# Optimization experiments

Hardware: AMD Instinct MI355X
Metric: run time of the kernel (lower is better)

The kernel has to match this reference:

```python
import jax, jax.numpy as jnp
import numpy as np
from jax import lax

B, C, TX, TY = 16, 192, 512, 2048
SEG = 8192 // 256  # segment_frames = 32 (hop length 256)
NEG_INF = -1e9


def setup_inputs() -> dict:
    key = jax.random.key(0)
    ks = jax.random.split(key, 7)
    z = jax.random.normal(ks[0], (B, C, TY), jnp.float32)
    z_p = jax.random.normal(ks[1], (B, C, TY), jnp.float32)
    m_p = jax.random.normal(ks[2], (B, C, TX), jnp.float32)
    logs_p = 0.1 * jax.random.normal(ks[3], (B, C, TX), jnp.float32)
    x_lengths = jax.random.randint(ks[4], (B,), TX // 2, TX + 1, jnp.int32)
    y_lengths = jax.random.randint(ks[5], (B,), TY // 2, TY + 1, jnp.int32)
    rand_u = jax.random.uniform(ks[6], (B,), jnp.float32)
    return dict(z=z, z_p=z_p, m_p=m_p, logs_p=logs_p,
                x_lengths=x_lengths, y_lengths=y_lengths, rand_u=rand_u)


def neg_cent_fn(z_p, m_p, logs_p):
    # sum_c -0.5 * exp(-2 logs)[c,tx] * (z_p[c,ty] - m_p[c,tx])^2 - sum_c logs[c,tx]
    # expanded (z-m)^2 = z^2 - 2 z m + m^2 -> batched GEMMs (same math as broadcast form)
    s = jnp.exp(-2.0 * logs_p)                                 # [B,C,Tx]
    a = jnp.einsum('bct,bcs->bts', -0.5 * z_p * z_p, s)        # [B,Ty,Tx]
    b = jnp.einsum('bct,bcs->bts', z_p, s * m_p)               # [B,Ty,Tx]
    c = jnp.sum(-0.5 * s * m_p * m_p - logs_p, axis=1)         # [B,Tx]
    return a + b + c[:, None, :]


def maximum_path_single(value, t_x, t_y):
    # Monotonic alignment search DP on value [Ty,Tx], valid region [:t_y,:t_x].
    Ty, Tx = value.shape
    tx = jnp.arange(Tx)

    def fwd(v, row):
        v_shift = jnp.concatenate([jnp.full((1,), NEG_INF, v.dtype), v[:-1]])
        dirn = v_shift > v                      # True: best predecessor is tx-1
        v_new = row + jnp.maximum(v, v_shift)
        v_new = jnp.where(tx < t_x, v_new, NEG_INF)
        v_new = jnp.maximum(v_new, NEG_INF)     # clamp accumulation
        return v_new, dirn

    v0 = jnp.where(tx == 0, 0.0, NEG_INF)
    _, dirs = lax.scan(fwd, v0, value)          # dirs [Ty,Tx] bool

    def bwd(idx, j):
        active = j < t_y
        idx = jnp.where(j == t_y - 1, t_x - 1, idx)
        row = jnp.where(active, jnp.zeros((Tx,), value.dtype).at[idx].set(1.0), 0.0)
        idx = jnp.where(active, idx - dirs[j, idx].astype(idx.dtype), idx)
        return idx, row

    _, path_rev = lax.scan(bwd, jnp.int32(0), jnp.arange(Ty - 1, -1, -1))
    return path_rev[::-1]                       # [Ty,Tx] 0/1 path


def rand_slice_segments(z, y_lengths, rand_u):
    t = z.shape[2]
    safe = jnp.minimum(y_lengths, t)
    ids_max = jnp.maximum(safe - SEG, 0)
    ids = (rand_u * (ids_max.astype(jnp.float32) + 1e-8)).astype(jnp.int32)
    zs = jax.vmap(lambda zi, s: lax.dynamic_slice_in_dim(zi, s, SEG, axis=1))(z, ids)
    valid = (jnp.arange(SEG)[None, None, :] < (safe - ids)[:, None, None])
    return zs * valid.astype(z.dtype), ids


def reference(z, z_p, m_p, logs_p, x_lengths, y_lengths, rand_u):
    neg_cent = neg_cent_fn(z_p, m_p, logs_p)                     # [B,Ty,Tx]
    attn = jax.vmap(maximum_path_single)(neg_cent, x_lengths, y_lengths)
    attn = lax.stop_gradient(attn)                               # torch: no_grad + detach
    m_p_a = jnp.einsum('bts,bcs->bct', attn, m_p)                # [B,C,Ty]
    logs_p_a = jnp.einsum('bts,bcs->bct', attn, logs_p)          # [B,C,Ty]
    z_slice, ids_slice = rand_slice_segments(z, y_lengths, rand_u)
    return z_slice, ids_slice, attn, m_p_a, logs_p_a
```

## Files before the change

### kernel.cpp

```cpp
#include <hip/hip_runtime.h>
#include <stdint.h>

#define B_   16
#define C_   192
#define TX_  512
#define TY_  2048
#define K_   384
#define SEG_ 32
#define NEG_INF_ (-1e9f)


__global__ __launch_bounds__(128) void k_prep(const float* __restrict__ mp,
                                              const float* __restrict__ logsp,
                                              float* __restrict__ Bmat,
                                              float* __restrict__ cterm) {
    int b  = blockIdx.y;
    int tx = blockIdx.x * 128 + threadIdx.x;
    const float* mb = mp    + (size_t)b * C_ * TX_ + tx;
    const float* lb = logsp + (size_t)b * C_ * TX_ + tx;
    float* B0 = Bmat + (size_t)b * K_ * TX_ + tx;
    float acc = 0.f;
    for (int c = 0; c < C_; ++c) {
        float lg = lb[(size_t)c * TX_];
        float m  = mb[(size_t)c * TX_];
        float s  = expf(-2.f * lg);
        B0[(size_t)c * TX_]        = s;
        B0[(size_t)(C_ + c) * TX_] = s * m;
        acc += -0.5f * s * m * m - lg;
    }
    cterm[b * TX_ + tx] = acc;
}

__global__ __launch_bounds__(256) void k_gemm(const float* __restrict__ zp,
                                              const float* __restrict__ Bmat,
                                              const float* __restrict__ cterm,
                                              float* __restrict__ ncout) {
    __shared__ float As[16][128];
    __shared__ float Bs[16][128];
    int b  = blockIdx.z;
    int m0 = blockIdx.y * 128;
    int n0 = blockIdx.x * 128;
    int tid = threadIdx.x;
    int tm = tid >> 4;
    int tn = tid & 15;
    const float* zpb = zp   + (size_t)b * C_ * TY_;
    const float* Bb  = Bmat + (size_t)b * K_ * TX_;

    float acc[8][8];
#pragma unroll
    for (int i = 0; i < 8; ++i)
#pragma unroll
        for (int j = 0; j < 8; ++j) acc[i][j] = 0.f;

    int lrow = tid >> 5;
    int lcol = (tid & 31) << 2;

    for (int k0 = 0; k0 < K_; k0 += 16) {
        int ksrc = (k0 < C_) ? k0 : (k0 - C_);
        const float* Ab = zpb + (size_t)(ksrc + lrow) * TY_ + m0 + lcol;
        float4 z0 = *(const float4*)Ab;
        float4 z1 = *(const float4*)(Ab + (size_t)8 * TY_);
        if (k0 < C_) {
            z0.x = -0.5f * z0.x * z0.x; z0.y = -0.5f * z0.y * z0.y;
            z0.z = -0.5f * z0.z * z0.z; z0.w = -0.5f * z0.w * z0.w;
            z1.x = -0.5f * z1.x * z1.x; z1.y = -0.5f * z1.y * z1.y;
            z1.z = -0.5f * z1.z * z1.z; z1.w = -0.5f * z1.w * z1.w;
        }
        const float* Bp = Bb + (size_t)(k0 + lrow) * TX_ + n0 + lcol;
        float4 w0 = *(const float4*)Bp;
        float4 w1 = *(const float4*)(Bp + (size_t)8 * TX_);

        __syncthreads();
        *(float4*)&As[lrow][lcol]     = z0;
        *(float4*)&As[lrow + 8][lcol] = z1;
        *(float4*)&Bs[lrow][lcol]     = w0;
        *(float4*)&Bs[lrow + 8][lcol] = w1;
        __syncthreads();

#pragma unroll
        for (int kk = 0; kk < 16; ++kk) {
            float4 a0 = *(const float4*)&As[kk][tm * 8];
            float4 a1 = *(const float4*)&As[kk][tm * 8 + 4];
            float4 b0 = *(const float4*)&Bs[kk][tn * 8];
            float4 b1 = *(const float4*)&Bs[kk][tn * 8 + 4];
            float a[8]  = {a0.x, a0.y, a0.z, a0.w, a1.x, a1.y, a1.z, a1.w};
            float bb[8] = {b0.x, b0.y, b0.z, b0.w, b1.x, b1.y, b1.z, b1.w};
#pragma unroll
            for (int i = 0; i < 8; ++i)
#pragma unroll
                for (int j = 0; j < 8; ++j)
                    acc[i][j] = fmaf(a[i], bb[j], acc[i][j]);
        }
    }

    float cadd[8];
#pragma unroll
    for (int j = 0; j < 8; ++j) cadd[j] = cterm[b * TX_ + n0 + tn * 8 + j];

#pragma unroll
    for (int i = 0; i < 8; ++i) {
        int row = m0 + tm * 8 + i;
        float* orow = ncout + ((size_t)b * TY_ + row) * TX_ + n0 + tn * 8;
        float4 o0, o1;
        o0.x = acc[i][0] + cadd[0]; o0.y = acc[i][1] + cadd[1];
        o0.z = acc[i][2] + cadd[2]; o0.w = acc[i][3] + cadd[3];
        o1.x = acc[i][4] + cadd[4]; o1.y = acc[i][5] + cadd[5];
        o1.z = acc[i][6] + cadd[6]; o1.w = acc[i][7] + cadd[7];
        *(float4*)orow       = o0;
        *(float4*)(orow + 4) = o1;
    }
}

#define NS_ 14
#define NP_ 7

__global__ __launch_bounds__(512, 1) void k_dp(const float* __restrict__ nc,
                                               const int* __restrict__ xl,
                                               const int* __restrict__ yl,
                                               int* __restrict__ path,
                                               unsigned char* __restrict__ gdirs) {
    extern __shared__ unsigned char slds[];
    float*    stagef   = (float*)slds;
    unsigned* flags    = (unsigned*)(slds + NS_ * 8192);
    unsigned* cons_ctr = flags + NS_;

    int b    = blockIdx.x;
    int tid  = threadIdx.x;
    int w    = tid >> 6;
    int lane = tid & 63;
    int t_x  = xl[b];
    int t_y  = yl[b]; if (t_y > TY_) t_y = TY_;
    const float* ncb = nc + (size_t)b * TY_ * TX_;
    unsigned char* gb = gdirs + (size_t)b * (TY_ * 64);
    int ng = (t_y + 3) >> 2;

    if (tid < NS_ + 1) flags[tid] = 0u;
    __syncthreads();

    if (w != 0) {
        int cv = (int)__hip_atomic_load(cons_ctr, __ATOMIC_ACQUIRE,
                                        __HIP_MEMORY_SCOPE_WORKGROUP);
        for (int g = w - 1; g < ng; g += NP_) {
            while (cv < g - (NS_ - 1)) {
                __builtin_amdgcn_s_sleep(1);
                cv = (int)__hip_atomic_load(cons_ctr, __ATOMIC_ACQUIRE,
                                            __HIP_MEMORY_SCOPE_WORKGROUP);
            }
            int j0 = g * 4;
            float* sb = stagef + (g % NS_) * 2048;
#pragma unroll
            for (int r = 0; r < 4; ++r) {
                const float4* row = (const float4*)(ncb + (size_t)(j0 + r) * TX_);
                float4 q0 = row[2 * lane];
                float4 q1 = row[2 * lane + 1];
                *(float4*)(sb + r * 512 + lane * 4)       = q0;
                *(float4*)(sb + r * 512 + 256 + lane * 4) = q1;
            }
            if (lane == 0)
                __hip_atomic_store(&flags[g % NS_], (unsigned)(g + 1),
                                   __ATOMIC_RELEASE, __HIP_MEMORY_SCOPE_WORKGROUP);
            cv = (int)__hip_atomic_load(cons_ctr, __ATOMIC_ACQUIRE,
                                        __HIP_MEMORY_SCOPE_WORKGROUP);
        }
        return;
    }

    int col0 = lane * 8;
    float v[8];
#pragma unroll
    for (int k = 0; k < 8; ++k) v[k] = (col0 + k == 0) ? 0.f : NEG_INF_;

    const unsigned neg_bits = __float_as_uint(NEG_INF_);
    unsigned fv = 0;
    for (int g = 0; g < ng; ++g) {
        while (fv != (unsigned)(g + 1))
            fv = __hip_atomic_load(&flags[g % NS_], __ATOMIC_ACQUIRE,
                                   __HIP_MEMORY_SCOPE_WORKGROUP);
        unsigned fnx = __hip_atomic_load(&flags[(g + 1) % NS_], __ATOMIC_ACQUIRE,
                                         __HIP_MEMORY_SCOPE_WORKGROUP);
        const float* rowp = stagef + (g % NS_) * 2048;
        unsigned dw = 0u;
#pragma unroll
        for (int r = 0; r < 4; ++r) {
            float4 p0 = *(const float4*)(rowp + r * 512 + lane * 4);
            float4 p1 = *(const float4*)(rowp + r * 512 + 256 + lane * 4);
            float rc[8] = {p0.x, p0.y, p0.z, p0.w, p1.x, p1.y, p1.z, p1.w};
            float left = __uint_as_float(__builtin_amdgcn_update_dpp(
                (int)neg_bits, (int)__float_as_uint(v[7]),
                0x138 , 0xF, 0xF, false));
            unsigned by = 0u;
#pragma unroll
            for (int k = 7; k >= 0; --k) {
                float vs = (k == 0) ? left : v[k - 1];
                if (vs > v[k]) by |= (1u << k);
                v[k] = fmaxf(v[k], vs) + rc[k];
            }
            dw |= by << (8 * r);
        }
        int j0 = g * 4;
        gb[(size_t)(j0    ) * 64 + lane] = (unsigned char)(dw      );
        gb[(size_t)(j0 + 1) * 64 + lane] = (unsigned char)(dw >>  8);
        gb[(size_t)(j0 + 2) * 64 + lane] = (unsigned char)(dw >> 16);
        gb[(size_t)(j0 + 3) * 64 + lane] = (unsigned char)(dw >> 24);
        if (lane == 0)
            __hip_atomic_store(cons_ctr, (unsigned)(g + 1),
                               __ATOMIC_RELEASE, __HIP_MEMORY_SCOPE_WORKGROUP);
        fv = fnx;
    }

    __builtin_amdgcn_s_waitcnt(3952);

    int* pb = path + b * TY_;
    for (int j2 = t_y + lane; j2 < TY_; j2 += 64) pb[j2] = -1;

    unsigned char* swin = (unsigned char*)stagef;
    int j   = t_y - 1;
    int idx = t_x - 1;
    while (j >= 0) {
        int nb = (j + 1 < 64) ? (j + 1) : 64;
        if (lane < nb) {
            const uint4* rp = (const uint4*)(gb + (size_t)(j - lane) * 64);
            uint4 a0 = rp[0], a1 = rp[1], a2 = rp[2], a3 = rp[3];
            uint4* wp = (uint4*)(swin + lane * 64);
            wp[0] = a0; wp[1] = a1; wp[2] = a2; wp[3] = a3;
        }
        if (lane == 0) {
            int r2 = 0;
            while (r2 < nb) {
                int n = nb - r2; if (n > 8) n = 8;
                int Bhi = idx >> 3;
                int Blo = Bhi - 1; if (Blo < 0) Blo = 0;
                unsigned lo8[8], hi8[8];
#pragma unroll
                for (int r = 0; r < 8; ++r) {
                    if (r < n) {
                        lo8[r] = swin[(r2 + r) * 64 + Blo];
                        hi8[r] = swin[(r2 + r) * 64 + Bhi];
                    }
                }
#pragma unroll
                for (int r = 0; r < 8; ++r) {
                    if (r < n) {
                        pb[j - (r2 + r)] = idx;
                        unsigned byte = ((idx >> 3) == Bhi) ? hi8[r] : lo8[r];
                        idx -= (int)((byte >> (idx & 7)) & 1u);
                    }
                }
                r2 += n;
            }
        }
        j -= nb;
    }
}

__global__ __launch_bounds__(256) void k_attn(const int* __restrict__ path,
                                              float* __restrict__ attn) {
    int i   = blockIdx.x * 256 + threadIdx.x;
    int tx0 = (i & 127) << 2;
    int bty = i >> 7;
    int p   = path[bty];
    float4 o;
    o.x = (p == tx0)     ? 1.f : 0.f;
    o.y = (p == tx0 + 1) ? 1.f : 0.f;
    o.z = (p == tx0 + 2) ? 1.f : 0.f;
    o.w = (p == tx0 + 3) ? 1.f : 0.f;
    ((float4*)attn)[i] = o;
}

__global__ __launch_bounds__(256) void k_proj(const int* __restrict__ path,
                                              const float* __restrict__ mp,
                                              const float* __restrict__ logsp,
                                              float* __restrict__ mpa,
                                              float* __restrict__ logsa) {
    int i   = blockIdx.x * 256 + threadIdx.x;
    int ty0 = (i & 511) << 2;
    int bc  = i >> 9;
    int b   = bc / C_;
    const int4 p4 = *(const int4*)(path + b * TY_ + ty0);
    const float* mrow = mp    + (size_t)bc * TX_;
    const float* lrow = logsp + (size_t)bc * TX_;
    float4 mo, lo;
    mo.x = (p4.x >= 0) ? mrow[p4.x] : 0.f;  lo.x = (p4.x >= 0) ? lrow[p4.x] : 0.f;
    mo.y = (p4.y >= 0) ? mrow[p4.y] : 0.f;  lo.y = (p4.y >= 0) ? lrow[p4.y] : 0.f;
    mo.z = (p4.z >= 0) ? mrow[p4.z] : 0.f;  lo.z = (p4.z >= 0) ? lrow[p4.z] : 0.f;
    mo.w = (p4.w >= 0) ? mrow[p4.w] : 0.f;  lo.w = (p4.w >= 0) ? lrow[p4.w] : 0.f;
    ((float4*)mpa)[i]   = mo;
    ((float4*)logsa)[i] = lo;
}

__global__ __launch_bounds__(256) void k_slice(const float* __restrict__ z,
                                               const int* __restrict__ yl,
                                               const float* __restrict__ ru,
                                               float* __restrict__ zs,
                                               float* __restrict__ oid) {
    int b = blockIdx.x;
    int safe = yl[b]; if (safe > TY_) safe = TY_;
    int idsmax = safe - SEG_; if (idsmax < 0) idsmax = 0;
    int ids = (int)(ru[b] * ((float)idsmax + 1e-8f));
    int lim = safe - ids;
    for (int t = threadIdx.x; t < C_ * SEG_; t += 256) {
        int c = t >> 5, k = t & 31;
        zs[b * C_ * SEG_ + t] =
            (k < lim) ? z[((size_t)b * C_ + c) * TY_ + ids + k] : 0.f;
    }
    if (threadIdx.x == 0) oid[b] = (float)ids;
}

extern "C" void kernel_launch(void* const* d_in, const int* in_sizes, int n_in,
                              void* d_out, int out_size, void* d_ws, size_t ws_size,
                              hipStream_t stream) {
    const float* z     = (const float*)d_in[0];
    const float* zp    = (const float*)d_in[1];
    const float* mp    = (const float*)d_in[2];
    const float* logsp = (const float*)d_in[3];
    const int*   xl    = (const int*)d_in[4];
    const int*   yl    = (const int*)d_in[5];
    const float* ru    = (const float*)d_in[6];

    float* out     = (float*)d_out;
    float* o_zs    = out;
    float* o_ids   = out + 98304;
    float* o_attn  = out + 98320;
    float* o_mpa   = out + 16875536;
    float* o_logsa = out + 23166992;

    float*         Bmat  = (float*)d_ws;
    float*         cterm = Bmat + (size_t)B_ * K_ * TX_;
    int*           path  = (int*)(cterm + B_ * TX_);
    unsigned char* gdirs = (unsigned char*)(path + B_ * TY_);

    const int dp_lds = NS_ * 8192 + 64;

    hipFuncSetAttribute((const void*)k_dp,
                        hipFuncAttributeMaxDynamicSharedMemorySize, dp_lds);

    hipLaunchKernelGGL(k_prep, dim3(TX_ / 128, B_), dim3(128), 0, stream,
                       mp, logsp, Bmat, cterm);
    hipLaunchKernelGGL(k_gemm, dim3(TX_ / 128, TY_ / 128, B_), dim3(256), 0, stream,
                       zp, Bmat, cterm, o_attn);
    hipLaunchKernelGGL(k_dp, dim3(B_), dim3(512), dp_lds, stream,
                       o_attn, xl, yl, path, gdirs);
    hipLaunchKernelGGL(k_attn, dim3(B_ * TY_ * TX_ / 4 / 256), dim3(256), 0, stream,
                       path, o_attn);
    hipLaunchKernelGGL(k_proj, dim3(B_ * C_ * TY_ / 4 / 256), dim3(256), 0, stream,
                       path, mp, logsp, o_mpa, o_logsa);
    hipLaunchKernelGGL(k_slice, dim3(B_), dim3(256), 0, stream,
                       z, yl, ru, o_zs, o_ids);
}
```

Measured before the change: 781.7 us.

## Replace flag-based DP staging ring with double-buffered phases and block barriers

The DP kernel's producer/consumer ring (14 slots, per-slot atomic flags, spin-waits) becomes a two-buffer scheme of 32-row phases, synchronised with __syncthreads. Producer waves fill the next 64 KB buffer while the consumer wave runs the DP recurrence on the current one. Direction bits are now stored as one 32-bit word per lane per 4 rows instead of four byte stores, and the backtrack window loads and addressing change to match. This removes fine-grained atomic polling and per-row byte stores, but the consumer now waits at a full barrier every 32 rows and LDS use rises to 128 KB.

```diff
diff --git a/kernel.cpp b/kernel.cpp
--- a/kernel.cpp
+++ b/kernel.cpp
@@ -111,18 +111,16 @@
     }
 }
 
-#define NS_ 14
-#define NP_ 7
+#define NPROD_ 7
 
 __global__ __launch_bounds__(512, 1) void k_dp(const float* __restrict__ nc,
                                                const int* __restrict__ xl,
                                                const int* __restrict__ yl,
                                                int* __restrict__ path,
-                                               unsigned char* __restrict__ gdirs) {
+                                               unsigned* __restrict__ gdirs32) {
     extern __shared__ unsigned char slds[];
-    float*    stagef   = (float*)slds;
-    unsigned* flags    = (unsigned*)(slds + NS_ * 8192);
-    unsigned* cons_ctr = flags + NS_;
+    float* buf0 = (float*)slds;
+    float* buf1 = (float*)(slds + 65536);
 
     int b    = blockIdx.x;
     int tid  = threadIdx.x;
@@ -131,36 +129,34 @@
     int t_x  = xl[b];
     int t_y  = yl[b]; if (t_y > TY_) t_y = TY_;
     const float* ncb = nc + (size_t)b * TY_ * TX_;
-    unsigned char* gb = gdirs + (size_t)b * (TY_ * 64);
-    int ng = (t_y + 3) >> 2;
-
-    if (tid < NS_ + 1) flags[tid] = 0u;
-    __syncthreads();
+    unsigned* gb32 = gdirs32 + (size_t)b * (TY_ / 4) * 64;
+    int nph = (t_y + 31) >> 5;
 
     if (w != 0) {
-        int cv = (int)__hip_atomic_load(cons_ctr, __ATOMIC_ACQUIRE,
-                                        __HIP_MEMORY_SCOPE_WORKGROUP);
-        for (int g = w - 1; g < ng; g += NP_) {
-            while (cv < g - (NS_ - 1)) {
-                __builtin_amdgcn_s_sleep(1);
-                cv = (int)__hip_atomic_load(cons_ctr, __ATOMIC_ACQUIRE,
-                                            __HIP_MEMORY_SCOPE_WORKGROUP);
-            }
-            int j0 = g * 4;
-            float* sb = stagef + (g % NS_) * 2048;
-#pragma unroll
-            for (int r = 0; r < 4; ++r) {
-                const float4* row = (const float4*)(ncb + (size_t)(j0 + r) * TX_);
+        {
+            for (int rr = w - 1; rr < 32; rr += NPROD_) {
+                const float4* row = (const float4*)(ncb + (size_t)rr * TX_);
                 float4 q0 = row[2 * lane];
                 float4 q1 = row[2 * lane + 1];
-                *(float4*)(sb + r * 512 + lane * 4)       = q0;
-                *(float4*)(sb + r * 512 + 256 + lane * 4) = q1;
+                *(float4*)(buf0 + rr * 512 + lane * 4)       = q0;
+                *(float4*)(buf0 + rr * 512 + 256 + lane * 4) = q1;
             }
-            if (lane == 0)
-                __hip_atomic_store(&flags[g % NS_], (unsigned)(g + 1),
-                                   __ATOMIC_RELEASE, __HIP_MEMORY_SCOPE_WORKGROUP);
-            cv = (int)__hip_atomic_load(cons_ctr, __ATOMIC_ACQUIRE,
-                                        __HIP_MEMORY_SCOPE_WORKGROUP);
+        }
+        __syncthreads();
+        for (int p = 0; p < nph; ++p) {
+            if (p + 1 < nph) {
+                float* sb = ((p + 1) & 1) ? buf1 : buf0;
+                int jbase = (p + 1) * 32;
+                for (int rr = w - 1; rr < 32; rr += NPROD_) {
+                    const float4* row =
+                        (const float4*)(ncb + (size_t)(jbase + rr) * TX_);
+                    float4 q0 = row[2 * lane];
+                    float4 q1 = row[2 * lane + 1];
+                    *(float4*)(sb + rr * 512 + lane * 4)       = q0;
+                    *(float4*)(sb + rr * 512 + 256 + lane * 4) = q1;
+                }
+            }
+            __syncthreads();
         }
         return;
     }
@@ -169,43 +165,35 @@
     float v[8];
 #pragma unroll
     for (int k = 0; k < 8; ++k) v[k] = (col0 + k == 0) ? 0.f : NEG_INF_;
-
     const unsigned neg_bits = __float_as_uint(NEG_INF_);
-    unsigned fv = 0;
-    for (int g = 0; g < ng; ++g) {
-        while (fv != (unsigned)(g + 1))
-            fv = __hip_atomic_load(&flags[g % NS_], __ATOMIC_ACQUIRE,
-                                   __HIP_MEMORY_SCOPE_WORKGROUP);
-        unsigned fnx = __hip_atomic_load(&flags[(g + 1) % NS_], __ATOMIC_ACQUIRE,
-                                         __HIP_MEMORY_SCOPE_WORKGROUP);
-        const float* rowp = stagef + (g % NS_) * 2048;
-        unsigned dw = 0u;
-#pragma unroll
-        for (int r = 0; r < 4; ++r) {
-            float4 p0 = *(const float4*)(rowp + r * 512 + lane * 4);
-            float4 p1 = *(const float4*)(rowp + r * 512 + 256 + lane * 4);
-            float rc[8] = {p0.x, p0.y, p0.z, p0.w, p1.x, p1.y, p1.z, p1.w};
-            float left = __uint_as_float(__builtin_amdgcn_update_dpp(
-                (int)neg_bits, (int)__float_as_uint(v[7]),
-                0x138 , 0xF, 0xF, false));
-            unsigned by = 0u;
-#pragma unroll
-            for (int k = 7; k >= 0; --k) {
-                float vs = (k == 0) ? left : v[k - 1];
-                if (vs > v[k]) by |= (1u << k);
-                v[k] = fmaxf(v[k], vs) + rc[k];
+
+    __syncthreads();
+    for (int p = 0; p < nph; ++p) {
+        const float* sb = (p & 1) ? buf1 : buf0;
+#pragma unroll
+        for (int g = 0; g < 8; ++g) {
+            unsigned dw = 0u;
+#pragma unroll
+            for (int r = 0; r < 4; ++r) {
+                const float* rowp = sb + (g * 4 + r) * 512;
+                float4 p0 = *(const float4*)(rowp + lane * 4);
+                float4 p1 = *(const float4*)(rowp + 256 + lane * 4);
+                float rc[8] = {p0.x, p0.y, p0.z, p0.w, p1.x, p1.y, p1.z, p1.w};
+                float left = __uint_as_float(__builtin_amdgcn_update_dpp(
+                    (int)neg_bits, (int)__float_as_uint(v[7]),
+                    0x138 , 0xF, 0xF, false));
+                unsigned by = 0u;
+#pragma unroll
+                for (int k = 7; k >= 0; --k) {
+                    float vs = (k == 0) ? left : v[k - 1];
+                    if (vs > v[k]) by |= (1u << k);
+                    v[k] = fmaxf(v[k], vs) + rc[k];
+                }
+                dw |= by << (8 * r);
             }
-            dw |= by << (8 * r);
-        }
-        int j0 = g * 4;
-        gb[(size_t)(j0    ) * 64 + lane] = (unsigned char)(dw      );
-        gb[(size_t)(j0 + 1) * 64 + lane] = (unsigned char)(dw >>  8);
-        gb[(size_t)(j0 + 2) * 64 + lane] = (unsigned char)(dw >> 16);
-        gb[(size_t)(j0 + 3) * 64 + lane] = (unsigned char)(dw >> 24);
-        if (lane == 0)
-            __hip_atomic_store(cons_ctr, (unsigned)(g + 1),
-                               __ATOMIC_RELEASE, __HIP_MEMORY_SCOPE_WORKGROUP);
-        fv = fnx;
+            gb32[(p * 8 + g) * 64 + lane] = dw;
+        }
+        __syncthreads();
     }
 
     __builtin_amdgcn_s_waitcnt(3952);
@@ -213,43 +201,49 @@
     int* pb = path + b * TY_;
     for (int j2 = t_y + lane; j2 < TY_; j2 += 64) pb[j2] = -1;
 
-    unsigned char* swin = (unsigned char*)stagef;
+    const unsigned char* gb = (const unsigned char*)gb32;
+    unsigned char* swin = (unsigned char*)buf0;
     int j   = t_y - 1;
     int idx = t_x - 1;
     while (j >= 0) {
-        int nb = (j + 1 < 64) ? (j + 1) : 64;
-        if (lane < nb) {
-            const uint4* rp = (const uint4*)(gb + (size_t)(j - lane) * 64);
-            uint4 a0 = rp[0], a1 = rp[1], a2 = rp[2], a3 = rp[3];
+        int wbase = (j & ~3) - 60; if (wbase < 0) wbase = 0;
+        {
+            const uint4* rp = (const uint4*)(gb + (size_t)(wbase >> 2) * 256);
+            uint4 a0 = rp[lane * 4 + 0];
+            uint4 a1 = rp[lane * 4 + 1];
+            uint4 a2 = rp[lane * 4 + 2];
+            uint4 a3 = rp[lane * 4 + 3];
             uint4* wp = (uint4*)(swin + lane * 64);
             wp[0] = a0; wp[1] = a1; wp[2] = a2; wp[3] = a3;
         }
         if (lane == 0) {
-            int r2 = 0;
-            while (r2 < nb) {
-                int n = nb - r2; if (n > 8) n = 8;
+            while (j >= wbase) {
+                int n = j - wbase + 1; if (n > 8) n = 8;
                 int Bhi = idx >> 3;
                 int Blo = Bhi - 1; if (Blo < 0) Blo = 0;
                 unsigned lo8[8], hi8[8];
 #pragma unroll
                 for (int r = 0; r < 8; ++r) {
                     if (r < n) {
-                        lo8[r] = swin[(r2 + r) * 64 + Blo];
-                        hi8[r] = swin[(r2 + r) * 64 + Bhi];
+                        int jr  = j - r;
+                        int off = ((jr - wbase) >> 2) * 256 + (jr & 3);
+                        lo8[r] = swin[off + Blo * 4];
+                        hi8[r] = swin[off + Bhi * 4];
                     }
                 }
 #pragma unroll
                 for (int r = 0; r < 8; ++r) {
                     if (r < n) {
-                        pb[j - (r2 + r)] = idx;
+                        pb[j - r] = idx;
                         unsigned byte = ((idx >> 3) == Bhi) ? hi8[r] : lo8[r];
                         idx -= (int)((byte >> (idx & 7)) & 1u);
                     }
                 }
-                r2 += n;
+                j -= n;
             }
         }
-        j -= nb;
+        j = wbase - 1;
+        j = __shfl(j, 0);
     }
 }
 
@@ -324,12 +318,12 @@
     float* o_mpa   = out + 16875536;
     float* o_logsa = out + 23166992;
 
-    float*         Bmat  = (float*)d_ws;
-    float*         cterm = Bmat + (size_t)B_ * K_ * TX_;
-    int*           path  = (int*)(cterm + B_ * TX_);
-    unsigned char* gdirs = (unsigned char*)(path + B_ * TY_);
-
-    const int dp_lds = NS_ * 8192 + 64;
+    float*    Bmat  = (float*)d_ws;
+    float*    cterm = Bmat + (size_t)B_ * K_ * TX_;
+    int*      path  = (int*)(cterm + B_ * TX_);
+    unsigned* gdirs = (unsigned*)(path + B_ * TY_);
+
+    const int dp_lds = 2 * 65536;
 
     hipFuncSetAttribute((const void*)k_dp,
                         hipFuncAttributeMaxDynamicSharedMemorySize, dp_lds);
```

Result: no change. 783.9 us (+0.3%).
